# Kernel optimization log

Measured on AMD Instinct MI355X. Metric: run time of the kernel, lower is better.

Reference implementation:

```python
import jax, jax.numpy as jnp
import numpy as np

PAD_IDX = 0


def setup_inputs() -> dict:
    key = jax.random.key(0)
    ks = jax.random.split(key, 8)
    B, S, V, E, H, O = 256, 512, 50000, 300, 50, 4
    tokens = jax.random.randint(ks[0], (B, S), 0, V, dtype=jnp.int32)
    emb_table = jax.random.normal(ks[1], (V, E), dtype=jnp.float32) * 0.1
    # zero the padding row, as torch nn.Embedding(padding_idx=0) does
    emb_table = emb_table.at[PAD_IDX].set(0.0)
    s_ih = 1.0 / np.sqrt(H)
    W_ih = jax.random.uniform(ks[2], (H, E), jnp.float32, -s_ih, s_ih)
    W_hh = jax.random.uniform(ks[3], (H, H), jnp.float32, -s_ih, s_ih)
    b_ih = jax.random.uniform(ks[4], (H,), jnp.float32, -s_ih, s_ih)
    b_hh = jax.random.uniform(ks[5], (H,), jnp.float32, -s_ih, s_ih)
    s_fc = 1.0 / np.sqrt(H)
    W_fc = jax.random.uniform(ks[6], (O, H), jnp.float32, -s_fc, s_fc)
    b_fc = jax.random.uniform(ks[7], (O,), jnp.float32, -s_fc, s_fc)
    return {"tokens": tokens, "emb_table": emb_table, "W_ih": W_ih,
            "W_hh": W_hh, "b_ih": b_ih, "b_hh": b_hh,
            "W_fc": W_fc, "b_fc": b_fc}


def reference(tokens, emb_table, W_ih, W_hh, b_ih, b_hh, W_fc, b_fc):
    B, S = tokens.shape
    H = W_hh.shape[0]
    # embedding lookup; mask padding rows (grad to pad row is blocked too)
    emb = emb_table[tokens]                      # [B,S,E]
    pad_mask = (tokens != PAD_IDX)[..., None]    # [B,S,1]
    emb = jnp.where(pad_mask, emb, 0.0)
    # input projection for all timesteps at once (big GEMM)
    x_proj = jnp.einsum("bse,he->bsh", emb, W_ih) + b_ih  # [B,S,H]
    # tanh recurrence: h_t = tanh(x_t + h_{t-1} @ W_hh^T + b_hh)
    h0 = jnp.zeros((B, H), dtype=emb.dtype)

    def step(h, x_t):
        h = jnp.tanh(x_t + h @ W_hh.T + b_hh)
        return h, None

    h_last, _ = jax.lax.scan(step, h0, jnp.swapaxes(x_proj, 0, 1))  # scan over S
    # final linear head on last hidden state
    return h_last @ W_fc.T + b_fc  # [B, O]
```

## Files before the change

kernel.cpp:

```cpp
#include <hip/hip_runtime.h>
#include <hip/hip_fp16.h>

#define PTAB_STRIDE 64

typedef float    f32x4 __attribute__((ext_vector_type(4)));
typedef _Float16 half8 __attribute__((ext_vector_type(8)));
typedef _Float16 h2    __attribute__((ext_vector_type(2)));

__device__ __forceinline__ h2 u2h2(unsigned int u) {
    union { unsigned int u; h2 h; } c; c.u = u; return c.h;
}

__device__ __forceinline__ float fdot2x(h2 a, h2 b, float c) {
#if __has_builtin(__builtin_amdgcn_fdot2)
    return __builtin_amdgcn_fdot2(a, b, c, false);
#else
    return c + (float)a[0] * (float)b[0] + (float)a[1] * (float)b[1];
#endif
}

__global__ __launch_bounds__(64) void prep_kernel(
    const float* __restrict__ Wih, const float* __restrict__ bih,
    const float* __restrict__ bhh, __half* __restrict__ Bfrag,
    float* __restrict__ bias64)
{
    const int lane = threadIdx.x;
    const int st   = blockIdx.x;
    if (st == 40) {
        if (lane < 64) bias64[lane] = (lane < 50) ? bih[lane] + bhh[lane] : 0.f;
        return;
    }
    const int s  = st >> 2, t = st & 3;
    const int n  = 16 * t + (lane & 15);
    const int kb = lane >> 4;
    half8 v;
    #pragma unroll
    for (int j = 0; j < 8; ++j) {
        const int k = 32 * s + 8 * kb + j;
        float w = 0.f;
        if (n < 50 && k < 300) w = Wih[n * 300 + k];
        v[j] = (_Float16)w;
    }
    *reinterpret_cast<half8*>(Bfrag + ((size_t)st * 64 + lane) * 8) = v;
}

__global__ __launch_bounds__(64) void ptab_mfma(
    const float* __restrict__ emb, const __half* __restrict__ Bfrag,
    const float* __restrict__ bias64, __half* __restrict__ ptab)
{
    const int lane = threadIdx.x;
    const int v0   = blockIdx.x * 16;
    const int m    = lane & 15;
    const int kb   = lane >> 4;
    const float* Erow = emb + (size_t)(v0 + m) * 300;
    const half8* BF   = reinterpret_cast<const half8*>(Bfrag);

    f32x4 acc[4];
    #pragma unroll
    for (int t = 0; t < 4; ++t) acc[t] = (f32x4){0.f, 0.f, 0.f, 0.f};

    #pragma unroll
    for (int s = 0; s < 9; ++s) {
        const int k0 = 32 * s + 8 * kb;
        float4 p0 = *(const float4*)(Erow + k0);
        float4 p1 = *(const float4*)(Erow + k0 + 4);
        half8 a;
        a[0] = (_Float16)p0.x; a[1] = (_Float16)p0.y;
        a[2] = (_Float16)p0.z; a[3] = (_Float16)p0.w;
        a[4] = (_Float16)p1.x; a[5] = (_Float16)p1.y;
        a[6] = (_Float16)p1.z; a[7] = (_Float16)p1.w;
        #pragma unroll
        for (int t = 0; t < 4; ++t)
            acc[t] = __builtin_amdgcn_mfma_f32_16x16x32_f16(
                a, BF[(4 * s + t) * 64 + lane], acc[t], 0, 0, 0);
    }
    {
        half8 a;
        #pragma unroll
        for (int j = 0; j < 8; ++j) {
            const int k = 288 + 8 * kb + j;
            float e = 0.f;
            if (k < 300) e = Erow[k];
            a[j] = (_Float16)e;
        }
        #pragma unroll
        for (int t = 0; t < 4; ++t)
            acc[t] = __builtin_amdgcn_mfma_f32_16x16x32_f16(
                a, BF[(36 + t) * 64 + lane], acc[t], 0, 0, 0);
    }

    const int nn = lane & 15;
    #pragma unroll
    for (int t = 0; t < 4; ++t) {
        const float bt = bias64[16 * t + nn];
        #pragma unroll
        for (int r = 0; r < 4; ++r)
            ptab[(size_t)(v0 + 4 * kb + r) * PTAB_STRIDE + 16 * t + nn] =
                (__half)(acc[t][r] + bt);
    }
}

__global__ __launch_bounds__(64, 1) void rnn_kernel(
    const int* __restrict__ tokens, const __half* __restrict__ ptab,
    const float* __restrict__ Whh,
    const float* __restrict__ Wfc, const float* __restrict__ bfc,
    float* __restrict__ out)
{
    __shared__ int stok[544];
    __shared__ __align__(16) _Float16 hbuf[64];
    const int lane = threadIdx.x;
    const int b    = blockIdx.x;
    const int hc   = lane < 50 ? lane : 49;

    #pragma unroll
    for (int k = 0; k < 8; ++k)
        stok[lane + 64 * k] = tokens[b * 512 + lane + 64 * k];
    if (lane < 32) stok[512 + lane] = 0;
    __syncthreads();

    unsigned int wh_u[25];
    #pragma unroll
    for (int j = 0; j < 25; ++j) {
        float2 w2 = *(const float2*)(Whh + hc * 50 + 2 * j);
        union { h2 h; unsigned int u; } c;
        c.h = (h2){(_Float16)w2.x, (_Float16)w2.y};
        wh_u[j] = c.u;
    }
    #pragma unroll
    for (int j = 0; j < 25; ++j)
        asm volatile("" : "+v"(wh_u[j]));

    float h = 0.f;

#define GA(T) ptab[(size_t)(T) * PTAB_STRIDE + lane]

    __half x0 = GA(stok[0]), x1 = GA(stok[1]), x2 = GA(stok[2]), x3 = GA(stok[3]);
    __half x4 = GA(stok[4]), x5 = GA(stok[5]), x6 = GA(stok[6]), x7 = GA(stok[7]);
    int k0 = stok[8],  k1 = stok[9],  k2 = stok[10], k3 = stok[11];
    int k4 = stok[12], k5 = stok[13], k6 = stok[14], k7 = stok[15];

#define SL(Q, i) __builtin_shufflevector(Q, Q, 2*(i), 2*(i)+1)
#define WH(j) u2h2(wh_u[j])

#define RNN_STEP(XV)                                                        \
    {                                                                       \
        hbuf[lane] = (_Float16)h;               \
        const half8* H8 = (const half8*)hbuf;                               \
        half8 q0 = H8[0], q1 = H8[1], q2 = H8[2];                           \
        half8 q3 = H8[3], q4 = H8[4], q5 = H8[5];                           \
        h2 q6 = *(const h2*)(hbuf + 48);                                    \
        float s0 = 0.f, s1 = 0.f;                                           \
        s0 = fdot2x(SL(q0,0), WH(0),  s0); s1 = fdot2x(SL(q0,1), WH(1),  s1); \
        s0 = fdot2x(SL(q0,2), WH(2),  s0); s1 = fdot2x(SL(q0,3), WH(3),  s1); \
        s0 = fdot2x(SL(q1,0), WH(4),  s0); s1 = fdot2x(SL(q1,1), WH(5),  s1); \
        s0 = fdot2x(SL(q1,2), WH(6),  s0); s1 = fdot2x(SL(q1,3), WH(7),  s1); \
        s0 = fdot2x(SL(q2,0), WH(8),  s0); s1 = fdot2x(SL(q2,1), WH(9),  s1); \
        s0 = fdot2x(SL(q2,2), WH(10), s0); s1 = fdot2x(SL(q2,3), WH(11), s1); \
        s0 = fdot2x(SL(q3,0), WH(12), s0); s1 = fdot2x(SL(q3,1), WH(13), s1); \
        s0 = fdot2x(SL(q3,2), WH(14), s0); s1 = fdot2x(SL(q3,3), WH(15), s1); \
        s0 = fdot2x(SL(q4,0), WH(16), s0); s1 = fdot2x(SL(q4,1), WH(17), s1); \
        s0 = fdot2x(SL(q4,2), WH(18), s0); s1 = fdot2x(SL(q4,3), WH(19), s1); \
        s0 = fdot2x(SL(q5,0), WH(20), s0); s1 = fdot2x(SL(q5,1), WH(21), s1); \
        s0 = fdot2x(SL(q5,2), WH(22), s0); s1 = fdot2x(SL(q5,3), WH(23), s1); \
        s0 = fdot2x(q6,       WH(24), s0);                                  \
        float a = (float)(XV) + (s0 + s1);                                  \
        a = fminf(9.f, fmaxf(-9.f, a));                                     \
        float e = __expf(2.f * a);                                          \
        h = fmaf(-2.f, __builtin_amdgcn_rcpf(e + 1.f), 1.f);                \
    }

    for (int t = 0; t < 512; t += 8) {
        __half n0 = GA(k0), n1 = GA(k1), n2 = GA(k2), n3 = GA(k3);
        __half n4 = GA(k4), n5 = GA(k5), n6 = GA(k6), n7 = GA(k7);
        k0 = stok[t + 16]; k1 = stok[t + 17]; k2 = stok[t + 18]; k3 = stok[t + 19];
        k4 = stok[t + 20]; k5 = stok[t + 21]; k6 = stok[t + 22]; k7 = stok[t + 23];

        RNN_STEP(x0); RNN_STEP(x1); RNN_STEP(x2); RNN_STEP(x3);
        RNN_STEP(x4); RNN_STEP(x5); RNN_STEP(x6); RNN_STEP(x7);

        x0 = n0; x1 = n1; x2 = n2; x3 = n3;
        x4 = n4; x5 = n5; x6 = n6; x7 = n7;
    }
#undef RNN_STEP
#undef SL
#undef WH
#undef GA

    float hv = (lane < 50) ? h : 0.f;
    #pragma unroll
    for (int o = 0; o < 4; ++o) {
        float w = (lane < 50) ? Wfc[o * 50 + lane] : 0.f;
        float p = hv * w;
        #pragma unroll
        for (int s = 32; s > 0; s >>= 1) p += __shfl_xor(p, s, 64);
        if (lane == 0) out[b * 4 + o] = p + bfc[o];
    }
}

extern "C" void kernel_launch(void* const* d_in, const int* in_sizes, int n_in,
                              void* d_out, int out_size, void* d_ws, size_t ws_size,
                              hipStream_t stream)
{
    const int*   tokens = (const int*)d_in[0];
    const float* emb    = (const float*)d_in[1];
    const float* Wih    = (const float*)d_in[2];
    const float* Whh    = (const float*)d_in[3];
    const float* bih    = (const float*)d_in[4];
    const float* bhh    = (const float*)d_in[5];
    const float* Wfc    = (const float*)d_in[6];
    const float* bfc    = (const float*)d_in[7];

    char* ws = (char*)d_ws;
    __half* ptab   = (__half*)ws;
    __half* Bfrag  = (__half*)(ws + 6400000);
    float*  bias64 = (float*)(ws + 6440960);
    float*  outp   = (float*)d_out;

    prep_kernel<<<41, 64, 0, stream>>>(Wih, bih, bhh, Bfrag, bias64);
    ptab_mfma<<<3125, 64, 0, stream>>>(emb, Bfrag, bias64, ptab);
    rnn_kernel<<<256, 64, 0, stream>>>(tokens, ptab, Whh, Wfc, bfc, outp);
}
```

Before: 110.6 us.

## Broadcast hidden state via DPP and permlane swaps instead of LDS round-trip

Each recurrence step no longer writes h to shared memory and reads it back. The hidden state is now distributed across lanes with DPP row shuffles and permlane16/32 swaps, so each lane gets all 64 values in register pairs. W_hh is pre-permuted per lane to match that lane-exchange pattern, which uses 32 packed registers instead of 25. The goal is to take LDS store/load latency off the serial dependency chain, at the cost of more cross-lane ops and fdot2 instructions per step (32 vs 25).

```diff
diff --git a/kernel.cpp b/kernel.cpp
--- a/kernel.cpp
+++ b/kernel.cpp
@@ -16,6 +16,41 @@
     return __builtin_amdgcn_fdot2(a, b, c, false);
 #else
     return c + (float)a[0] * (float)b[0] + (float)a[1] * (float)b[1];
+#endif
+}
+
+#if __has_builtin(__builtin_amdgcn_permlane16_swap)
+#define HAVE_PL16 1
+#else
+#define HAVE_PL16 0
+#endif
+#if __has_builtin(__builtin_amdgcn_permlane32_swap)
+#define HAVE_PL32 1
+#else
+#define HAVE_PL32 0
+#endif
+
+#define DPPX(v, ctrl) \
+    ((unsigned)__builtin_amdgcn_update_dpp(0, (int)(v), (ctrl), 0xf, 0xf, true))
+
+__device__ __forceinline__ void xsw16(unsigned p, unsigned &A, unsigned &B) {
+#if HAVE_PL16
+    auto rr = __builtin_amdgcn_permlane16_swap(p, p, false, false);
+    A = (unsigned)rr[0]; B = (unsigned)rr[1];
+#else
+    A = p;
+    B = (unsigned)__builtin_amdgcn_ds_swizzle((int)p, 0x401F);
+#endif
+}
+
+__device__ __forceinline__ void xsw32(unsigned x, unsigned &P, unsigned &Q) {
+#if HAVE_PL32
+    auto rr = __builtin_amdgcn_permlane32_swap(x, x, false, false);
+    P = (unsigned)rr[0]; Q = (unsigned)rr[1];
+#else
+    P = x;
+    Q = (unsigned)__builtin_amdgcn_ds_bpermute(
+            (int)(((threadIdx.x ^ 32) & 63) << 2), (int)x);
 #endif
 }
 
@@ -107,10 +142,8 @@
     float* __restrict__ out)
 {
     __shared__ int stok[544];
-    __shared__ __align__(16) _Float16 hbuf[64];
     const int lane = threadIdx.x;
     const int b    = blockIdx.x;
-    const int hc   = lane < 50 ? lane : 49;
 
     #pragma unroll
     for (int k = 0; k < 8; ++k)
@@ -118,17 +151,34 @@
     if (lane < 32) stok[512 + lane] = 0;
     __syncthreads();
 
-    unsigned int wh_u[25];
-    #pragma unroll
-    for (int j = 0; j < 25; ++j) {
-        float2 w2 = *(const float2*)(Whh + hc * 50 + 2 * j);
-        union { h2 h; unsigned int u; } c;
-        c.h = (h2){(_Float16)w2.x, (_Float16)w2.y};
-        wh_u[j] = c.u;
-    }
-    #pragma unroll
-    for (int j = 0; j < 25; ++j)
-        asm volatile("" : "+v"(wh_u[j]));
+    const int mA16 = HAVE_PL16 ? ((lane & 16) ? 16 : 0) : 0;
+    const int mB16 = HAVE_PL16 ? ((lane & 16) ? 0 : 16) : 16;
+    const int aP32 = HAVE_PL32 ? ((lane & 32) ? 32 : 0) : 0;
+    const int aQ32 = HAVE_PL32 ? ((lane & 32) ? 0 : 32) : 32;
+    const int mfam[4] = {mA16 | aP32, mA16 | aQ32, mB16 | aP32, mB16 | aQ32};
+    const int dlt[8]  = {0, 2, 7, 5, 15, 13, 8, 10};
+
+    unsigned wpk[8][4];
+    #pragma unroll
+    for (int di = 0; di < 8; ++di) {
+        #pragma unroll
+        for (int f = 0; f < 4; ++f) {
+            const int ka = lane ^ dlt[di] ^ mfam[f];
+            const int kb = ka ^ 1;
+            _Float16 wa = (lane < 50 && ka < 50)
+                              ? (_Float16)Whh[lane * 50 + ka] : (_Float16)0.f;
+            _Float16 wb = (lane < 50 && kb < 50)
+                              ? (_Float16)Whh[lane * 50 + kb] : (_Float16)0.f;
+            union { h2 h; unsigned u; } c;
+            c.h = (h2){wa, wb};
+            wpk[di][f] = c.u;
+        }
+    }
+    #pragma unroll
+    for (int di = 0; di < 8; ++di)
+        #pragma unroll
+        for (int f = 0; f < 4; ++f)
+            asm volatile("" : "+v"(wpk[di][f]));
 
     float h = 0.f;
 
@@ -139,34 +189,44 @@
     int k0 = stok[8],  k1 = stok[9],  k2 = stok[10], k3 = stok[11];
     int k4 = stok[12], k5 = stok[13], k6 = stok[14], k7 = stok[15];
 
-#define SL(Q, i) __builtin_shufflevector(Q, Q, 2*(i), 2*(i)+1)
-#define WH(j) u2h2(wh_u[j])
-
-#define RNN_STEP(XV)                                                        \
-    {                                                                       \
-        hbuf[lane] = (_Float16)h;               \
-        const half8* H8 = (const half8*)hbuf;                               \
-        half8 q0 = H8[0], q1 = H8[1], q2 = H8[2];                           \
-        half8 q3 = H8[3], q4 = H8[4], q5 = H8[5];                           \
-        h2 q6 = *(const h2*)(hbuf + 48);                                    \
-        float s0 = 0.f, s1 = 0.f;                                           \
-        s0 = fdot2x(SL(q0,0), WH(0),  s0); s1 = fdot2x(SL(q0,1), WH(1),  s1); \
-        s0 = fdot2x(SL(q0,2), WH(2),  s0); s1 = fdot2x(SL(q0,3), WH(3),  s1); \
-        s0 = fdot2x(SL(q1,0), WH(4),  s0); s1 = fdot2x(SL(q1,1), WH(5),  s1); \
-        s0 = fdot2x(SL(q1,2), WH(6),  s0); s1 = fdot2x(SL(q1,3), WH(7),  s1); \
-        s0 = fdot2x(SL(q2,0), WH(8),  s0); s1 = fdot2x(SL(q2,1), WH(9),  s1); \
-        s0 = fdot2x(SL(q2,2), WH(10), s0); s1 = fdot2x(SL(q2,3), WH(11), s1); \
-        s0 = fdot2x(SL(q3,0), WH(12), s0); s1 = fdot2x(SL(q3,1), WH(13), s1); \
-        s0 = fdot2x(SL(q3,2), WH(14), s0); s1 = fdot2x(SL(q3,3), WH(15), s1); \
-        s0 = fdot2x(SL(q4,0), WH(16), s0); s1 = fdot2x(SL(q4,1), WH(17), s1); \
-        s0 = fdot2x(SL(q4,2), WH(18), s0); s1 = fdot2x(SL(q4,3), WH(19), s1); \
-        s0 = fdot2x(SL(q5,0), WH(20), s0); s1 = fdot2x(SL(q5,1), WH(21), s1); \
-        s0 = fdot2x(SL(q5,2), WH(22), s0); s1 = fdot2x(SL(q5,3), WH(23), s1); \
-        s0 = fdot2x(q6,       WH(24), s0);                                  \
-        float a = (float)(XV) + (s0 + s1);                                  \
-        a = fminf(9.f, fmaxf(-9.f, a));                                     \
-        float e = __expf(2.f * a);                                          \
-        h = fmaf(-2.f, __builtin_amdgcn_rcpf(e + 1.f), 1.f);                \
+#define RNN_STEP(XV)                                                         \
+    {                                                                        \
+        union { _Float16 hf; unsigned short us; } hcv;                       \
+        hcv.hf = (_Float16)h;                                                \
+        unsigned hh = hcv.us;                                                \
+        unsigned nb = DPPX(hh, 0xB1);                              \
+        unsigned p  = hh | (nb << 16);                                       \
+        unsigned A, B;                                                       \
+        xsw16(p, A, B);                                           \
+        unsigned g[8][4];                                                    \
+        xsw32(A, g[0][0], g[0][1]);                               \
+        xsw32(B, g[0][2], g[0][3]);                                          \
+        _Pragma("unroll")                                                    \
+        for (int f = 0; f < 4; ++f)                                          \
+            g[1][f] = DPPX(g[0][f], 0x4E);                         \
+        _Pragma("unroll")                                                    \
+        for (int f = 0; f < 4; ++f) {                                        \
+            g[2][f] = DPPX(g[0][f], 0x141);                        \
+            g[3][f] = DPPX(g[1][f], 0x141);                                  \
+        }                                                                    \
+        _Pragma("unroll")                                                    \
+        for (int f = 0; f < 4; ++f) {                                        \
+            g[4][f] = DPPX(g[0][f], 0x140);                       \
+            g[5][f] = DPPX(g[1][f], 0x140);                                  \
+            g[6][f] = DPPX(g[2][f], 0x140);                                  \
+            g[7][f] = DPPX(g[3][f], 0x140);                                  \
+        }                                                                    \
+        float s[4] = {0.f, 0.f, 0.f, 0.f};                                   \
+        _Pragma("unroll")                                                    \
+        for (int di = 0; di < 8; ++di) {                                     \
+            _Pragma("unroll")                                                \
+            for (int f = 0; f < 4; ++f)                                      \
+                s[f] = fdot2x(u2h2(g[di][f]), u2h2(wpk[di][f]), s[f]);       \
+        }                                                                    \
+        float a = (float)(XV) + ((s[0] + s[1]) + (s[2] + s[3]));             \
+        a = fminf(9.f, fmaxf(-9.f, a));                                      \
+        float e = __expf(2.f * a);                                           \
+        h = fmaf(-2.f, __builtin_amdgcn_rcpf(e + 1.f), 1.f);                 \
     }
 
     for (int t = 0; t < 512; t += 8) {
@@ -182,8 +242,6 @@
         x4 = n4; x5 = n5; x6 = n6; x7 = n7;
     }
 #undef RNN_STEP
-#undef SL
-#undef WH
 #undef GA
 
     float hv = (lane < 50) ? h : 0.f;
```

New measurement: 130.7 us. 1.18x slower.

## Broadcast hidden state via DPP and permlane swaps instead of LDS

Applied to the files above, without the earlier changes.

Replaces the per-step LDS store and reload of the fp16 hidden vector with in-register cross-lane exchange. It packs neighbour pairs with DPP, spreads them with permlane16/32 swaps and row-rotation DPPs, and pre-permutes the W_hh weights to match each lane's rotated view. The aim is to remove LDS latency from the serial recurrence critical path, at the cost of about 30 DPP ops per step and 32 dot products instead of 25. It relies on gfx950 permlane swap instructions and correct DPP control encodings.

```diff
diff --git a/kernel.cpp b/kernel.cpp
--- a/kernel.cpp
+++ b/kernel.cpp
@@ -16,6 +16,31 @@
     return __builtin_amdgcn_fdot2(a, b, c, false);
 #else
     return c + (float)a[0] * (float)b[0] + (float)a[1] * (float)b[1];
+#endif
+}
+
+#define DPPX(v, ctrl) \
+    ((unsigned)__builtin_amdgcn_update_dpp(0, (int)(v), (ctrl), 0xf, 0xf, true))
+
+__device__ __forceinline__ void swap16(unsigned &a, unsigned &b) {
+#if __has_builtin(__builtin_amdgcn_permlane16_swap)
+    auto rr = __builtin_amdgcn_permlane16_swap(a, b, false, false);
+    a = (unsigned)rr[0]; b = (unsigned)rr[1];
+#else
+    asm volatile("s_nop 1\n\t"
+                 "v_permlane16_swap_b32 %0, %1"
+                 : "+v"(a), "+v"(b));
+#endif
+}
+
+__device__ __forceinline__ void swap32(unsigned &a, unsigned &b) {
+#if __has_builtin(__builtin_amdgcn_permlane32_swap)
+    auto rr = __builtin_amdgcn_permlane32_swap(a, b, false, false);
+    a = (unsigned)rr[0]; b = (unsigned)rr[1];
+#else
+    asm volatile("s_nop 1\n\t"
+                 "v_permlane32_swap_b32 %0, %1"
+                 : "+v"(a), "+v"(b));
 #endif
 }
 
@@ -107,10 +132,8 @@
     float* __restrict__ out)
 {
     __shared__ int stok[544];
-    __shared__ __align__(16) _Float16 hbuf[64];
     const int lane = threadIdx.x;
     const int b    = blockIdx.x;
-    const int hc   = lane < 50 ? lane : 49;
 
     #pragma unroll
     for (int k = 0; k < 8; ++k)
@@ -118,17 +141,26 @@
     if (lane < 32) stok[512 + lane] = 0;
     __syncthreads();
 
-    unsigned int wh_u[25];
-    #pragma unroll
-    for (int j = 0; j < 25; ++j) {
-        float2 w2 = *(const float2*)(Whh + hc * 50 + 2 * j);
-        union { h2 h; unsigned int u; } c;
-        c.h = (h2){(_Float16)w2.x, (_Float16)w2.y};
-        wh_u[j] = c.u;
-    }
-    #pragma unroll
-    for (int j = 0; j < 25; ++j)
-        asm volatile("" : "+v"(wh_u[j]));
+    const int lb = lane & 15;
+    const int base[4] = {lb, lb | 32, lb | 16, lb | 48};
+    const int dlt[8]  = {0, 2, 7, 5, 15, 13, 8, 10};
+
+    unsigned wpk[8][4];
+    #pragma unroll
+    for (int di = 0; di < 8; ++di) {
+        #pragma unroll
+        for (int f = 0; f < 4; ++f) {
+            const int ka = base[f] ^ dlt[di];
+            const int kb2 = ka ^ 1;
+            _Float16 wa = (lane < 50 && ka < 50)
+                              ? (_Float16)Whh[lane * 50 + ka]  : (_Float16)0.f;
+            _Float16 wb = (lane < 50 && kb2 < 50)
+                              ? (_Float16)Whh[lane * 50 + kb2] : (_Float16)0.f;
+            union { h2 h; unsigned u; } c;
+            c.h = (h2){wa, wb};
+            wpk[di][f] = c.u;
+        }
+    }
 
     float h = 0.f;
 
@@ -139,34 +171,50 @@
     int k0 = stok[8],  k1 = stok[9],  k2 = stok[10], k3 = stok[11];
     int k4 = stok[12], k5 = stok[13], k6 = stok[14], k7 = stok[15];
 
-#define SL(Q, i) __builtin_shufflevector(Q, Q, 2*(i), 2*(i)+1)
-#define WH(j) u2h2(wh_u[j])
-
-#define RNN_STEP(XV)                                                        \
-    {                                                                       \
-        hbuf[lane] = (_Float16)h;               \
-        const half8* H8 = (const half8*)hbuf;                               \
-        half8 q0 = H8[0], q1 = H8[1], q2 = H8[2];                           \
-        half8 q3 = H8[3], q4 = H8[4], q5 = H8[5];                           \
-        h2 q6 = *(const h2*)(hbuf + 48);                                    \
-        float s0 = 0.f, s1 = 0.f;                                           \
-        s0 = fdot2x(SL(q0,0), WH(0),  s0); s1 = fdot2x(SL(q0,1), WH(1),  s1); \
-        s0 = fdot2x(SL(q0,2), WH(2),  s0); s1 = fdot2x(SL(q0,3), WH(3),  s1); \
-        s0 = fdot2x(SL(q1,0), WH(4),  s0); s1 = fdot2x(SL(q1,1), WH(5),  s1); \
-        s0 = fdot2x(SL(q1,2), WH(6),  s0); s1 = fdot2x(SL(q1,3), WH(7),  s1); \
-        s0 = fdot2x(SL(q2,0), WH(8),  s0); s1 = fdot2x(SL(q2,1), WH(9),  s1); \
-        s0 = fdot2x(SL(q2,2), WH(10), s0); s1 = fdot2x(SL(q2,3), WH(11), s1); \
-        s0 = fdot2x(SL(q3,0), WH(12), s0); s1 = fdot2x(SL(q3,1), WH(13), s1); \
-        s0 = fdot2x(SL(q3,2), WH(14), s0); s1 = fdot2x(SL(q3,3), WH(15), s1); \
-        s0 = fdot2x(SL(q4,0), WH(16), s0); s1 = fdot2x(SL(q4,1), WH(17), s1); \
-        s0 = fdot2x(SL(q4,2), WH(18), s0); s1 = fdot2x(SL(q4,3), WH(19), s1); \
-        s0 = fdot2x(SL(q5,0), WH(20), s0); s1 = fdot2x(SL(q5,1), WH(21), s1); \
-        s0 = fdot2x(SL(q5,2), WH(22), s0); s1 = fdot2x(SL(q5,3), WH(23), s1); \
-        s0 = fdot2x(q6,       WH(24), s0);                                  \
-        float a = (float)(XV) + (s0 + s1);                                  \
-        a = fminf(9.f, fmaxf(-9.f, a));                                     \
-        float e = __expf(2.f * a);                                          \
-        h = fmaf(-2.f, __builtin_amdgcn_rcpf(e + 1.f), 1.f);                \
+#define DOT4(di, V0, V1, V2, V3)                                             \
+        s0 = fdot2x(u2h2(V0), u2h2(wpk[di][0]), s0);                         \
+        s1 = fdot2x(u2h2(V1), u2h2(wpk[di][1]), s1);                         \
+        s2 = fdot2x(u2h2(V2), u2h2(wpk[di][2]), s2);                         \
+        s3 = fdot2x(u2h2(V3), u2h2(wpk[di][3]), s3);
+
+#define RNN_STEP(XV)                                                         \
+    {                                                                        \
+        union { _Float16 hf; unsigned short us; } hcv;                       \
+        hcv.hf = (_Float16)h;                                                \
+        unsigned hh = (unsigned)hcv.us;                                      \
+        unsigned nbr = DPPX(hh, 0xB1);                             \
+        unsigned p   = hh | (nbr << 16);                 \
+        unsigned a16 = p, b16 = p;                                           \
+        swap16(a16, b16);                                                    \
+        unsigned F0 = a16, F1 = a16; swap32(F0, F1);                         \
+        unsigned F2 = b16, F3 = b16; swap32(F2, F3);                         \
+        float s0 = 0.f, s1 = 0.f, s2 = 0.f, s3 = 0.f;                        \
+        DOT4(0, F0, F1, F2, F3)                                    \
+        unsigned A0 = DPPX(F0, 0x4E), A1 = DPPX(F1, 0x4E);                   \
+        unsigned A2 = DPPX(F2, 0x4E), A3 = DPPX(F3, 0x4E);                   \
+        DOT4(1, A0, A1, A2, A3)                                    \
+        unsigned B0 = DPPX(F0, 0x141), B1 = DPPX(F1, 0x141);                 \
+        unsigned B2 = DPPX(F2, 0x141), B3 = DPPX(F3, 0x141);                 \
+        DOT4(2, B0, B1, B2, B3)                                    \
+        unsigned C0 = DPPX(A0, 0x141), C1 = DPPX(A1, 0x141);                 \
+        unsigned C2 = DPPX(A2, 0x141), C3 = DPPX(A3, 0x141);                 \
+        DOT4(3, C0, C1, C2, C3)                                    \
+        unsigned D0 = DPPX(F0, 0x140), D1 = DPPX(F1, 0x140);                 \
+        unsigned D2 = DPPX(F2, 0x140), D3 = DPPX(F3, 0x140);                 \
+        DOT4(4, D0, D1, D2, D3)                                    \
+        unsigned E0 = DPPX(A0, 0x140), E1 = DPPX(A1, 0x140);                 \
+        unsigned E2 = DPPX(A2, 0x140), E3 = DPPX(A3, 0x140);                 \
+        DOT4(5, E0, E1, E2, E3)                                    \
+        unsigned G0 = DPPX(B0, 0x140), G1 = DPPX(B1, 0x140);                 \
+        unsigned G2 = DPPX(B2, 0x140), G3 = DPPX(B3, 0x140);                 \
+        DOT4(6, G0, G1, G2, G3)                                    \
+        unsigned H0 = DPPX(C0, 0x140), H1 = DPPX(C1, 0x140);                 \
+        unsigned H2 = DPPX(C2, 0x140), H3 = DPPX(C3, 0x140);                 \
+        DOT4(7, H0, H1, H2, H3)                                    \
+        float aa = (float)(XV) + ((s0 + s1) + (s2 + s3));                    \
+        aa = fminf(9.f, fmaxf(-9.f, aa));                                    \
+        float ee = __expf(2.f * aa);                                         \
+        h = fmaf(-2.f, __builtin_amdgcn_rcpf(ee + 1.f), 1.f);                \
     }
 
     for (int t = 0; t < 512; t += 8) {
@@ -182,8 +230,7 @@
         x4 = n4; x5 = n5; x6 = n6; x7 = n7;
     }
 #undef RNN_STEP
-#undef SL
-#undef WH
+#undef DOT4
 #undef GA
 
     float hv = (lane < 50) ? h : 0.f;
```

New measurement: 133.2 us. +20.5%, slower.
